# Performance work log

Measured on AMD Instinct MI355X. Metric: run time of the kernel, lower is better.

The kernel has to match this reference:

```python
import jax, jax.numpy as jnp
import numpy as np

B, T, D = 2, 2048, 1024
H, HD = 16, 64
MAX_LEN = 2048


def setup_inputs() -> dict:
    key = jax.random.key(0)
    ks = jax.random.split(key, 7)
    s = 0.02
    return {
        "x": jax.random.normal(ks[0], (B, T, D), dtype=jnp.float32),
        "qkv_w": jax.random.normal(ks[1], (3 * D, D), dtype=jnp.float32) * s,
        "qkv_b": jax.random.normal(ks[2], (3 * D,), dtype=jnp.float32) * s,
        "out_w": jax.random.normal(ks[3], (D, D), dtype=jnp.float32) * s,
        "out_b": jax.random.normal(ks[4], (D,), dtype=jnp.float32) * s,
        "rel_pos": jax.random.normal(ks[5], (2 * MAX_LEN - 1, HD), dtype=jnp.float32),
        "rpe_w": jax.random.normal(ks[6], (HD,), dtype=jnp.float32) * s,
    }


def reference(x, qkv_w, qkv_b, out_w, out_b, rel_pos, rpe_w):
    Bq, Tq, Dq = x.shape
    scale = HD ** -0.5
    qkv = x @ qkv_w.T + qkv_b  # [B,T,3D]
    qkv = qkv.reshape(Bq, Tq, 3, H, HD)
    q = qkv[:, :, 0].transpose(0, 2, 1, 3)  # [B,H,T,HD]
    k = qkv[:, :, 1].transpose(0, 2, 1, 3)
    v = qkv[:, :, 2].transpose(0, 2, 1, 3)
    scores = jnp.einsum('bhqd,bhkd->bhqk', q, k) * scale  # [B,H,T,T]
    # relative position bias: gather rel embeddings, project to scalar
    rel_idx = jnp.arange(Tq)[None, :] - jnp.arange(Tq)[:, None] + MAX_LEN - 1  # [T,T]
    bias = (rel_pos @ rpe_w)[rel_idx]  # project first (cheap), then gather -> [T,T]
    scores = scores + bias[None, None]
    attn = jax.nn.softmax(scores, axis=-1)
    out = jnp.einsum('bhqk,bhkd->bhqd', attn, v)  # [B,H,T,HD]
    out = out.transpose(0, 2, 1, 3).reshape(Bq, Tq, Dq)
    return out @ out_w.T + out_b
```

## Files before the change

### kernel.cpp

```cpp
#include <hip/hip_runtime.h>
#include <math.h>

#define B_ 2
#define T_ 2048
#define D_ 1024
#define H_ 16
#define HD_ 64
#define MAXLEN_ 2048
#define N3D_ 3072
#define M_ (B_ * T_)
#define KA 1024

#define SCALE_L2E 0.18033688011116215f
#define L2E 1.4426950408889634f

typedef unsigned short ushort_t;
typedef __attribute__((ext_vector_type(8))) short short8;
typedef __attribute__((ext_vector_type(4))) float floatx4;
#define MFMA16(a, b, c) __builtin_amdgcn_mfma_f32_16x16x32_bf16(a, b, c, 0, 0, 0)

static __device__ __forceinline__ ushort_t f2bf(float f) {
    unsigned u = __float_as_uint(f);
    unsigned r = (u + 0x7FFFu + ((u >> 16) & 1u)) >> 16;
    return (ushort_t)r;
}
static __device__ __forceinline__ unsigned packrnu(float a, float b) {
    unsigned ua = __float_as_uint(a) + 0x8000u;
    unsigned ub = __float_as_uint(b) + 0x8000u;
    return __builtin_amdgcn_perm(ub, ua, 0x07060302u);
}

static __device__ __forceinline__ void gld16(const ushort_t* g, ushort_t* l) {
    __builtin_amdgcn_global_load_lds(
        (const __attribute__((address_space(1))) void*)g,
        (__attribute__((address_space(3))) void*)l, 16, 0, 0);
}

__global__ __launch_bounds__(256) void cvt_all(
    const float* __restrict__ x, const float* __restrict__ qw,
    const float* __restrict__ ow, const float* __restrict__ rel_pos,
    const float* __restrict__ rpe_w,
    ushort_t* __restrict__ Xc, ushort_t* __restrict__ QWc,
    ushort_t* __restrict__ OWc, float* __restrict__ biasp)
{
    const int row = blockIdx.x;
    if (row < M_ + N3D_ + D_) {
        const float* src; ushort_t* dst; int r;
        if (row < M_)            { src = x;  dst = Xc;  r = row; }
        else if (row < M_ + N3D_){ src = qw; dst = QWc; r = row - M_; }
        else                     { src = ow; dst = OWc; r = row - M_ - N3D_; }
        const int c = threadIdx.x * 4;
        float4 v = *(const float4*)(src + (size_t)r * 1024 + c);
        ushort4 hv;
        hv.x = f2bf(v.x); hv.y = f2bf(v.y); hv.z = f2bf(v.z); hv.w = f2bf(v.w);
        *(ushort4*)(dst + (size_t)r * KA + c) = hv;
    } else {
        const int wv = threadIdx.x >> 6, lane = threadIdx.x & 63;
        const int r = (row - (M_ + N3D_ + D_)) * 4 + wv;
        if (r < 2 * MAXLEN_ - 1) {
            float v = rel_pos[(size_t)r * HD_ + lane] * rpe_w[lane];
#pragma unroll
            for (int off = 32; off; off >>= 1) v += __shfl_down(v, off);
            if (lane == 0) biasp[r] = v * L2E;
        }
    }
}

__global__ __launch_bounds__(512, 2) void qkv_mfma(
    const ushort_t* __restrict__ Ac, const ushort_t* __restrict__ Bc,
    const float* __restrict__ bias,
    ushort_t* __restrict__ Qs, ushort_t* __restrict__ Khi,
    ushort_t* __restrict__ Vt)
{
    __shared__ __align__(16) ushort_t LDS[2][2][32 * 512];

    const int tid = threadIdx.x;
    const int wv = tid >> 6, lane = tid & 63;
    const int l16 = lane & 15, quad = lane >> 4;
    const int wr = wv >> 2, wc = wv & 3;

    const int orig = blockIdx.y * 12 + blockIdx.x;
    const int swz = (orig & 7) * 24 + (orig >> 3);
    const int m0 = (swz / 12) * 256, n0 = (swz % 12) * 256;

    floatx4 acc[8][4];
#pragma unroll
    for (int i = 0; i < 8; ++i)
#pragma unroll
        for (int j = 0; j < 4; ++j) acc[i][j] = (floatx4){0.f, 0.f, 0.f, 0.f};

    short8 af[4][2];
    short8 bf[2][2][2];

#define BARX() asm volatile("s_barrier" ::: "memory")
#define WAITVM(n) asm volatile("s_waitcnt vmcnt(" #n ")" ::: "memory")

#define STAGE(bufi, ab, unit, tile) do {                                      \
    const ushort_t* _src = (ab) ? Bc : Ac;                                    \
    const int _rc = (ab) ? n0 : m0;                                           \
    const int _I = (unit) * 8 + wv;                                           \
    const ushort_t* _g = _src + (size_t)(_rc + _I * 16 + l16) * KA            \
                              + ((tile) * 64 + quad * 8);                     \
    ushort_t* _l = &LDS[bufi][ab][(_I * 2) * 512];                            \
    gld16(_g, _l);                                                            \
    gld16(_g + 32, _l + 512);                                                 \
} while (0)

#define RD_AF(bufi, mi) do {                                                  \
    _Pragma("unroll") for (int ii = 0; ii < 4; ++ii) {                        \
        const int _I = wr * 8 + (mi) * 4 + ii;                                \
        af[ii][0] = *(const short8*)(&LDS[bufi][0][(_I * 2 + 0) * 512] + lane * 8); \
        af[ii][1] = *(const short8*)(&LDS[bufi][0][(_I * 2 + 1) * 512] + lane * 8); \
    } } while (0)

#define RD_BF(bufi, ni) do {                                                  \
    _Pragma("unroll") for (int jj = 0; jj < 2; ++jj) {                        \
        const int _I = wc * 4 + (ni) * 2 + jj;                                \
        bf[ni][jj][0] = *(const short8*)(&LDS[bufi][1][(_I * 2 + 0) * 512] + lane * 8); \
        bf[ni][jj][1] = *(const short8*)(&LDS[bufi][1][(_I * 2 + 1) * 512] + lane * 8); \
    } } while (0)

#define MM(mi, ni) do {                                                       \
    __builtin_amdgcn_s_setprio(1);                                            \
    _Pragma("unroll") for (int ii = 0; ii < 4; ++ii)                          \
    _Pragma("unroll") for (int jj = 0; jj < 2; ++jj) {                        \
        acc[(mi)*4+ii][(ni)*2+jj] = MFMA16(af[ii][0], bf[ni][jj][0], acc[(mi)*4+ii][(ni)*2+jj]); \
        acc[(mi)*4+ii][(ni)*2+jj] = MFMA16(af[ii][1], bf[ni][jj][1], acc[(mi)*4+ii][(ni)*2+jj]); \
    }                                                                         \
    __builtin_amdgcn_s_setprio(0);                                            \
} while (0)

    STAGE(0, 1, 0, 0); STAGE(0, 1, 1, 0);
    STAGE(0, 0, 0, 0); STAGE(0, 0, 1, 0);
    STAGE(1, 1, 0, 1); STAGE(1, 1, 1, 1);
    WAITVM(4);
    BARX();

#pragma unroll 1
    for (int j = 0; j < 8; ++j) {
        const int tY  = 2 * j + 1;
        const int tX2 = (2 * j + 2) & 15;
        const int tY2 = (2 * j + 3) & 15;
        RD_AF(0, 0); RD_BF(0, 0); STAGE(1, 0, 0, tY);  BARX(); MM(0, 0); BARX();
        RD_BF(0, 1);              STAGE(1, 0, 1, tY);  BARX(); MM(0, 1); BARX();
        RD_AF(0, 1);              STAGE(0, 1, 0, tX2); BARX(); MM(1, 0); BARX();
                                  STAGE(0, 1, 1, tX2); BARX(); MM(1, 1);
        WAITVM(4); BARX();
        RD_AF(1, 0); RD_BF(1, 0); STAGE(0, 0, 0, tX2); BARX(); MM(0, 0); BARX();
        RD_BF(1, 1);              STAGE(0, 0, 1, tX2); BARX(); MM(0, 1); BARX();
        RD_AF(1, 1);              STAGE(1, 1, 0, tY2); BARX(); MM(1, 0); BARX();
                                  STAGE(1, 1, 1, tY2); BARX(); MM(1, 1);
        WAITVM(4); BARX();
    }

#undef BARX
#undef WAITVM
#undef STAGE
#undef RD_AF
#undef RD_BF
#undef MM

#pragma unroll
    for (int mi = 0; mi < 8; ++mi) {
#pragma unroll
        for (int r = 0; r < 4; ++r) {
            const int m = m0 + wr * 128 + mi * 16 + quad * 4 + r;
            const int bb = m >> 11, t = m & 2047;
#pragma unroll
            for (int jj = 0; jj < 4; ++jj) {
                const int n = n0 + wc * 64 + jj * 16 + l16;
                const int c = n >> 10, h = (n >> 6) & 15, hd = n & 63;
                const float v = acc[mi][jj][r] + bias[n];
                const size_t idx = (((size_t)bb * H_ + h) * T_ + t) * HD_ + hd;
                if (c == 0) { Qs[idx] = f2bf(v * SCALE_L2E); }
                else if (c == 1) { Khi[idx] = f2bf(v); }
                else { Vt[(((size_t)bb * H_ + h) * HD_ + hd) * T_ + t] = f2bf(v); }
            }
        }
    }
}

__global__ __launch_bounds__(256) void out_mfma(
    const ushort_t* __restrict__ Ac, const ushort_t* __restrict__ Bc,
    const float* __restrict__ bias, float* __restrict__ Out)
{
    __shared__ __align__(16) ushort_t As[2][16 * 512];
    __shared__ __align__(16) ushort_t Bs[2][8 * 512];
    const int tid = threadIdx.x;
    const int wv = tid >> 6, lane = tid & 63;
    const int l16 = lane & 15, quad = lane >> 4;
    const int wm = wv & 1, wn = wv >> 1;

    const int orig = blockIdx.y * 16 + blockIdx.x;
    const int swz = (orig & 7) * 64 + (orig >> 3);
    const int m0 = (swz >> 4) * 128, n0 = (swz & 15) * 64;

    floatx4 acc[4][2];
#pragma unroll
    for (int i = 0; i < 4; ++i)
#pragma unroll
        for (int j = 0; j < 2; ++j) acc[i][j] = (floatx4){0.f, 0.f, 0.f, 0.f};

    auto stage = [&](int bufi, int kk) {
#pragma unroll
        for (int c = 0; c < 4; ++c) {
            const int b = wv * 4 + c;
            const int i = b >> 1, ks = b & 1;
            const int k = kk + ks * 32 + quad * 8;
            gld16(Ac + (size_t)(m0 + i * 16 + l16) * KA + k, As[bufi] + b * 512);
        }
#pragma unroll
        for (int c = 0; c < 2; ++c) {
            const int b = wv * 2 + c;
            const int j = b >> 1, ks = b & 1;
            const int k = kk + ks * 32 + quad * 8;
            gld16(Bc + (size_t)(n0 + j * 16 + l16) * KA + k, Bs[bufi] + b * 512);
        }
    };

    stage(0, 0);
    __syncthreads();

#pragma unroll 1
    for (int t = 0; t < 16; ++t) {
        const int cur = t & 1;
        if (t < 15) stage(cur ^ 1, (t + 1) * 64);
#pragma unroll
        for (int ks = 0; ks < 2; ++ks) {
            short8 af[4], bf[2];
#pragma unroll
            for (int ii = 0; ii < 4; ++ii)
                af[ii] = *(const short8*)(As[cur] + ((wm * 4 + ii) * 2 + ks) * 512 + lane * 8);
#pragma unroll
            for (int jj = 0; jj < 2; ++jj)
                bf[jj] = *(const short8*)(Bs[cur] + ((wn * 2 + jj) * 2 + ks) * 512 + lane * 8);
#pragma unroll
            for (int ii = 0; ii < 4; ++ii)
#pragma unroll
                for (int jj = 0; jj < 2; ++jj)
                    acc[ii][jj] = MFMA16(af[ii], bf[jj], acc[ii][jj]);
        }
        if (t < 15) __syncthreads();
    }

#pragma unroll
    for (int ii = 0; ii < 4; ++ii) {
#pragma unroll
        for (int r = 0; r < 4; ++r) {
            const int m = m0 + wm * 64 + ii * 16 + quad * 4 + r;
#pragma unroll
            for (int jj = 0; jj < 2; ++jj) {
                const int n = n0 + wn * 32 + jj * 16 + l16;
                Out[(size_t)m * D_ + n] = acc[ii][jj][r] + bias[n];
            }
        }
    }
}

__global__ __launch_bounds__(256, 4) void attn_mfma(
    const ushort_t* __restrict__ Qs, const ushort_t* __restrict__ Khi,
    const ushort_t* __restrict__ Vt, const float* __restrict__ biasp,
    ushort_t* __restrict__ AOc)
{
    __shared__ __align__(16) ushort_t KS[2][8 * 512];
    __shared__ __align__(16) ushort_t VS[2][8 * 512];
    __shared__ __align__(16) ushort_t PS[4][1024];

    const int i = blockIdx.x;
    const int j = i >> 3;
    const int bh = (i & 7) + 8 * (j >> 5);
    const int q0 = (j & 31) * 64;
    const int tid = threadIdx.x;
    const int wv = tid >> 6, lane = tid & 63;
    const int l16 = lane & 15, quad = lane >> 4;

    const int qw = q0 + wv * 16;

    short8 qh[2];
    {
        const size_t qoff = ((size_t)bh * T_ + qw + l16) * HD_ + quad * 8;
        qh[0] = *(const short8*)(Qs + qoff);
        qh[1] = *(const short8*)(Qs + qoff + 32);
    }

    float l_r = 0.f;
    floatx4 o_acc[4];
#pragma unroll
    for (int g2 = 0; g2 < 4; ++g2) o_acc[g2] = (floatx4){0.f, 0.f, 0.f, 0.f};

    const ushort_t* gK = Khi + (size_t)bh * T_ * HD_;
    const ushort_t* gV = Vt + (size_t)bh * HD_ * T_;
    const int c0base = 2047 + quad * 4 - (qw + l16);

    const size_t kstage = (size_t)(wv * 16 + l16) * HD_ + quad * 8;
    const size_t vstage = (size_t)(wv * 16 + l16) * T_ + quad * 8;

    gld16(gK + kstage,      KS[0] + (wv * 2 + 0) * 512);
    gld16(gK + kstage + 32, KS[0] + (wv * 2 + 1) * 512);
    gld16(gV + vstage,      VS[0] + (wv * 2 + 0) * 512);
    gld16(gV + vstage + 32, VS[0] + (wv * 2 + 1) * 512);
    __syncthreads();

#define PSW(u) ((u) ^ ((((u) >> 6) & 3) << 4))

    for (int t = 0; t < 32; ++t) {
        const int k0 = t * 64;
        const int buf = t & 1, nbuf = buf ^ 1;

        float4 f4[4];
        {
            const float* bp = biasp + (c0base + k0);
#pragma unroll
            for (int z = 0; z < 4; ++z)
                __builtin_memcpy(&f4[z], bp + z * 16, 16);
        }

        if (t < 31) {
            const size_t koff = kstage + (size_t)(k0 + 64) * HD_;
            gld16(gK + koff,      KS[nbuf] + (wv * 2 + 0) * 512);
            gld16(gK + koff + 32, KS[nbuf] + (wv * 2 + 1) * 512);
            const size_t voff = vstage + (size_t)(k0 + 64);
            gld16(gV + voff,      VS[nbuf] + (wv * 2 + 0) * 512);
            gld16(gV + voff + 32, VS[nbuf] + (wv * 2 + 1) * 512);
        }

#pragma unroll
        for (int g = 0; g < 4; ++g) {
            const short8 kh0 = *(const short8*)(KS[buf] + (g * 2 + 0) * 512 + lane * 8);
            const short8 kh1 = *(const short8*)(KS[buf] + (g * 2 + 1) * 512 + lane * 8);
            const float4 bbv = f4[g];
            floatx4 a = (floatx4){bbv.x, bbv.y, bbv.z, bbv.w};
            a = MFMA16(kh0, qh[0], a);
            a = MFMA16(kh1, qh[1], a);
            const float p0 = __builtin_amdgcn_exp2f(a[0]);
            const float p1 = __builtin_amdgcn_exp2f(a[1]);
            const float p2 = __builtin_amdgcn_exp2f(a[2]);
            const float p3 = __builtin_amdgcn_exp2f(a[3]);
            l_r += (p0 + p1) + (p2 + p3);
            uint2 pkd;
            pkd.x = packrnu(p0, p1);
            pkd.y = packrnu(p2, p3);
            const int qd = 2 * (g & 1) + (quad >> 1);
            const int widx = (g >> 1) * 512 + (qd * 16 + l16) * 8 + (quad & 1) * 4;
            *(uint2*)(PS[wv] + PSW(widx)) = pkd;
        }

        short8 pf[2];
        {
            const int r0 = lane * 8, r1 = 512 + lane * 8;
            pf[0] = *(const short8*)(PS[wv] + PSW(r0));
            pf[1] = *(const short8*)(PS[wv] + PSW(r1));
        }

#pragma unroll
        for (int g2 = 0; g2 < 4; ++g2) {
            const short8 v0 = *(const short8*)(VS[buf] + (g2 * 2 + 0) * 512 + lane * 8);
            const short8 v1 = *(const short8*)(VS[buf] + (g2 * 2 + 1) * 512 + lane * 8);
            o_acc[g2] = MFMA16(v0, pf[0], o_acc[g2]);
            o_acc[g2] = MFMA16(v1, pf[1], o_acc[g2]);
        }
        __syncthreads();
    }

#undef PSW

    const int bb2 = bh >> 4, h2 = bh & 15;
    l_r += __shfl_xor(l_r, 16);
    l_r += __shfl_xor(l_r, 32);
    const float inv = 1.0f / l_r;
    const size_t m = (size_t)bb2 * T_ + qw + l16;
#pragma unroll
    for (int g2 = 0; g2 < 4; ++g2) {
        uint2 pk;
        pk.x = packrnu(o_acc[g2][0] * inv, o_acc[g2][1] * inv);
        pk.y = packrnu(o_acc[g2][2] * inv, o_acc[g2][3] * inv);
        *(uint2*)(AOc + m * KA + h2 * 64 + g2 * 16 + quad * 4) = pk;
    }
}

extern "C" void kernel_launch(void* const* d_in, const int* in_sizes, int n_in,
                              void* d_out, int out_size, void* d_ws, size_t ws_size,
                              hipStream_t stream)
{
    const float* x       = (const float*)d_in[0];
    const float* qkv_w   = (const float*)d_in[1];
    const float* qkv_b   = (const float*)d_in[2];
    const float* out_w   = (const float*)d_in[3];
    const float* out_b   = (const float*)d_in[4];
    const float* rel_pos = (const float*)d_in[5];
    const float* rpe_w   = (const float*)d_in[6];
    float* out = (float*)d_out;

    const size_t QE = (size_t)B_ * H_ * T_ * HD_;
    ushort_t* Qs  = (ushort_t*)d_ws;
    ushort_t* Khi = Qs  + QE;
    ushort_t* Vt  = Khi + QE;
    ushort_t* Xc  = Vt  + QE;
    ushort_t* QWc = Xc  + (size_t)M_ * KA;
    ushort_t* OWc = QWc + (size_t)N3D_ * KA;
    ushort_t* AOc = OWc + (size_t)D_ * KA;
    float* biasp  = (float*)(AOc + (size_t)M_ * KA);

    cvt_all<<<M_ + N3D_ + D_ + 1024, 256, 0, stream>>>(
        x, qkv_w, out_w, rel_pos, rpe_w, Xc, QWc, OWc, biasp);

    qkv_mfma<<<dim3(12, 16), 512, 0, stream>>>(
        Xc, QWc, qkv_b, Qs, Khi, Vt);
    attn_mfma<<<1024, 256, 0, stream>>>(Qs, Khi, Vt, biasp, AOc);
    out_mfma<<<dim3(D_ / 64, M_ / 128), 256, 0, stream>>>(
        AOc, OWc, out_b, out);
}
```

Baseline: 255.7 us.

## Split attention keys across waves, keep P in registers, reduce partials via LDS

The attention kernel now has each wave process all 64 queries of the block against its own 16-key slice of every 64-key tile. Its K and V fragments are loaded straight from global memory into registers, so the LDS staging buffers and per-iteration barriers are gone. The exp'd probabilities are fed directly as a zero-padded MFMA operand instead of a round trip through LDS. Per-wave partial outputs and row sums are combined through shared memory at the end. This wastes half of each PV MFMA on zero padding, raises register pressure (launch bounds drop to 3 blocks), and issues uncoalesced direct global loads with no prefetch overlap.

Result: slower. 329.6 us (+28.9%).

```diff
diff --git a/kernel.cpp b/kernel.cpp
--- a/kernel.cpp
+++ b/kernel.cpp
@@ -28,6 +28,11 @@
     unsigned ua = __float_as_uint(a) + 0x8000u;
     unsigned ub = __float_as_uint(b) + 0x8000u;
     return __builtin_amdgcn_perm(ub, ua, 0x07060302u);
+}
+static __device__ __forceinline__ short8 lo8(unsigned a, unsigned b) {
+    union { unsigned u[4]; short8 s; } x;
+    x.u[0] = a; x.u[1] = b; x.u[2] = 0; x.u[3] = 0;
+    return x.s;
 }
 
 static __device__ __forceinline__ void gld16(const ushort_t* g, ushort_t* l) {
@@ -257,14 +262,14 @@
     }
 }
 
-__global__ __launch_bounds__(256, 4) void attn_mfma(
+__global__ __launch_bounds__(256, 3) void attn_mfma(
     const ushort_t* __restrict__ Qs, const ushort_t* __restrict__ Khi,
     const ushort_t* __restrict__ Vt, const float* __restrict__ biasp,
     ushort_t* __restrict__ AOc)
 {
-    __shared__ __align__(16) ushort_t KS[2][8 * 512];
-    __shared__ __align__(16) ushort_t VS[2][8 * 512];
-    __shared__ __align__(16) ushort_t PS[4][1024];
+    __shared__ __align__(16) float ored[4][64][16];
+    __shared__ float lred[4][64];
+    __shared__ float linv[64];
 
     const int i = blockIdx.x;
     const int j = i >> 3;
@@ -274,107 +279,91 @@
     const int wv = tid >> 6, lane = tid & 63;
     const int l16 = lane & 15, quad = lane >> 4;
 
-    const int qw = q0 + wv * 16;
-
-    short8 qh[2];
-    {
-        const size_t qoff = ((size_t)bh * T_ + qw + l16) * HD_ + quad * 8;
-        qh[0] = *(const short8*)(Qs + qoff);
-        qh[1] = *(const short8*)(Qs + qoff + 32);
-    }
-
-    float l_r = 0.f;
-    floatx4 o_acc[4];
-#pragma unroll
-    for (int g2 = 0; g2 < 4; ++g2) o_acc[g2] = (floatx4){0.f, 0.f, 0.f, 0.f};
-
-    const ushort_t* gK = Khi + (size_t)bh * T_ * HD_;
-    const ushort_t* gV = Vt + (size_t)bh * HD_ * T_;
-    const int c0base = 2047 + quad * 4 - (qw + l16);
-
-    const size_t kstage = (size_t)(wv * 16 + l16) * HD_ + quad * 8;
-    const size_t vstage = (size_t)(wv * 16 + l16) * T_ + quad * 8;
-
-    gld16(gK + kstage,      KS[0] + (wv * 2 + 0) * 512);
-    gld16(gK + kstage + 32, KS[0] + (wv * 2 + 1) * 512);
-    gld16(gV + vstage,      VS[0] + (wv * 2 + 0) * 512);
-    gld16(gV + vstage + 32, VS[0] + (wv * 2 + 1) * 512);
-    __syncthreads();
-
-#define PSW(u) ((u) ^ ((((u) >> 6) & 3) << 4))
-
+    short8 qh[4][2];
+#pragma unroll
+    for (int qg = 0; qg < 4; ++qg) {
+        const size_t qoff = ((size_t)bh * T_ + q0 + qg * 16 + l16) * HD_ + quad * 8;
+        qh[qg][0] = *(const short8*)(Qs + qoff);
+        qh[qg][1] = *(const short8*)(Qs + qoff + 32);
+    }
+
+    floatx4 o_acc[4][4];
+#pragma unroll
+    for (int dg = 0; dg < 4; ++dg)
+#pragma unroll
+        for (int qg = 0; qg < 4; ++qg) o_acc[dg][qg] = (floatx4){0.f, 0.f, 0.f, 0.f};
+    float l_r[4] = {0.f, 0.f, 0.f, 0.f};
+
+    const ushort_t* kptr = Khi + ((size_t)bh * T_ + wv * 16 + l16) * HD_ + quad * 8;
+    const ushort_t* vptr = Vt + (size_t)bh * HD_ * T_ + (size_t)l16 * T_ + wv * 16 + quad * 4;
+    const float* bbase = biasp + (2047 + wv * 16 + quad * 4 - q0 - l16);
+
+#pragma unroll 1
     for (int t = 0; t < 32; ++t) {
         const int k0 = t * 64;
-        const int buf = t & 1, nbuf = buf ^ 1;
-
+        const short8 kc0 = *(const short8*)(kptr + (size_t)k0 * HD_);
+        const short8 kc1 = *(const short8*)(kptr + (size_t)k0 * HD_ + 32);
+        short8 vf[4];
+#pragma unroll
+        for (int dg = 0; dg < 4; ++dg) {
+            const uint2 vv = *(const uint2*)(vptr + (size_t)(dg * 16) * T_ + k0);
+            vf[dg] = lo8(vv.x, vv.y);
+        }
         float4 f4[4];
-        {
-            const float* bp = biasp + (c0base + k0);
-#pragma unroll
-            for (int z = 0; z < 4; ++z)
-                __builtin_memcpy(&f4[z], bp + z * 16, 16);
-        }
-
-        if (t < 31) {
-            const size_t koff = kstage + (size_t)(k0 + 64) * HD_;
-            gld16(gK + koff,      KS[nbuf] + (wv * 2 + 0) * 512);
-            gld16(gK + koff + 32, KS[nbuf] + (wv * 2 + 1) * 512);
-            const size_t voff = vstage + (size_t)(k0 + 64);
-            gld16(gV + voff,      VS[nbuf] + (wv * 2 + 0) * 512);
-            gld16(gV + voff + 32, VS[nbuf] + (wv * 2 + 1) * 512);
-        }
-
-#pragma unroll
-        for (int g = 0; g < 4; ++g) {
-            const short8 kh0 = *(const short8*)(KS[buf] + (g * 2 + 0) * 512 + lane * 8);
-            const short8 kh1 = *(const short8*)(KS[buf] + (g * 2 + 1) * 512 + lane * 8);
-            const float4 bbv = f4[g];
-            floatx4 a = (floatx4){bbv.x, bbv.y, bbv.z, bbv.w};
-            a = MFMA16(kh0, qh[0], a);
-            a = MFMA16(kh1, qh[1], a);
+#pragma unroll
+        for (int qg = 0; qg < 4; ++qg)
+            __builtin_memcpy(&f4[qg], bbase + k0 - qg * 16, 16);
+
+#pragma unroll
+        for (int qg = 0; qg < 4; ++qg) {
+            floatx4 a = (floatx4){f4[qg].x, f4[qg].y, f4[qg].z, f4[qg].w};
+            a = MFMA16(kc0, qh[qg][0], a);
+            a = MFMA16(kc1, qh[qg][1], a);
             const float p0 = __builtin_amdgcn_exp2f(a[0]);
             const float p1 = __builtin_amdgcn_exp2f(a[1]);
             const float p2 = __builtin_amdgcn_exp2f(a[2]);
             const float p3 = __builtin_amdgcn_exp2f(a[3]);
-            l_r += (p0 + p1) + (p2 + p3);
-            uint2 pkd;
-            pkd.x = packrnu(p0, p1);
-            pkd.y = packrnu(p2, p3);
-            const int qd = 2 * (g & 1) + (quad >> 1);
-            const int widx = (g >> 1) * 512 + (qd * 16 + l16) * 8 + (quad & 1) * 4;
-            *(uint2*)(PS[wv] + PSW(widx)) = pkd;
-        }
-
-        short8 pf[2];
-        {
-            const int r0 = lane * 8, r1 = 512 + lane * 8;
-            pf[0] = *(const short8*)(PS[wv] + PSW(r0));
-            pf[1] = *(const short8*)(PS[wv] + PSW(r1));
-        }
-
-#pragma unroll
-        for (int g2 = 0; g2 < 4; ++g2) {
-            const short8 v0 = *(const short8*)(VS[buf] + (g2 * 2 + 0) * 512 + lane * 8);
-            const short8 v1 = *(const short8*)(VS[buf] + (g2 * 2 + 1) * 512 + lane * 8);
-            o_acc[g2] = MFMA16(v0, pf[0], o_acc[g2]);
-            o_acc[g2] = MFMA16(v1, pf[1], o_acc[g2]);
-        }
+            l_r[qg] += (p0 + p1) + (p2 + p3);
+            const short8 pb = lo8(packrnu(p0, p1), packrnu(p2, p3));
+#pragma unroll
+            for (int dg = 0; dg < 4; ++dg)
+                o_acc[dg][qg] = MFMA16(vf[dg], pb, o_acc[dg][qg]);
+        }
+    }
+
+#pragma unroll
+    for (int qg = 0; qg < 4; ++qg) {
+        l_r[qg] += __shfl_xor(l_r[qg], 16);
+        l_r[qg] += __shfl_xor(l_r[qg], 32);
+    }
+    if (quad == 0) {
+#pragma unroll
+        for (int qg = 0; qg < 4; ++qg) lred[wv][qg * 16 + l16] = l_r[qg];
+    }
+    __syncthreads();
+    if (tid < 64)
+        linv[tid] = 1.0f / (lred[0][tid] + lred[1][tid] + lred[2][tid] + lred[3][tid]);
+
+    const int bb2 = bh >> 4, h2 = bh & 15;
+    const int rq = tid >> 2, rd = (tid & 3) * 4;
+#pragma unroll 1
+    for (int dg = 0; dg < 4; ++dg) {
         __syncthreads();
-    }
-
-#undef PSW
-
-    const int bb2 = bh >> 4, h2 = bh & 15;
-    l_r += __shfl_xor(l_r, 16);
-    l_r += __shfl_xor(l_r, 32);
-    const float inv = 1.0f / l_r;
-    const size_t m = (size_t)bb2 * T_ + qw + l16;
-#pragma unroll
-    for (int g2 = 0; g2 < 4; ++g2) {
+#pragma unroll
+        for (int qg = 0; qg < 4; ++qg)
+            *(floatx4*)&ored[wv][qg * 16 + l16][quad * 4] = o_acc[dg][qg];
+        __syncthreads();
+        floatx4 s = *(const floatx4*)&ored[0][rq][rd];
+#pragma unroll
+        for (int w = 1; w < 4; ++w) {
+            const floatx4 sw = *(const floatx4*)&ored[w][rq][rd];
+            s[0] += sw[0]; s[1] += sw[1]; s[2] += sw[2]; s[3] += sw[3];
+        }
+        const float iv = linv[rq];
         uint2 pk;
-        pk.x = packrnu(o_acc[g2][0] * inv, o_acc[g2][1] * inv);
-        pk.y = packrnu(o_acc[g2][2] * inv, o_acc[g2][3] * inv);
-        *(uint2*)(AOc + m * KA + h2 * 64 + g2 * 16 + quad * 4) = pk;
+        pk.x = packrnu(s[0] * iv, s[1] * iv);
+        pk.y = packrnu(s[2] * iv, s[3] * iv);
+        *(uint2*)(AOc + ((size_t)bb2 * T_ + q0 + rq) * KA + h2 * 64 + dg * 16 + rd) = pk;
     }
 }
 
```
